# Optimization experiments

Measured on AMD Instinct MI355X. Metric: run time of the kernel, lower is better.

The kernel has to match this reference:

```python
import jax, jax.numpy as jnp
import numpy as np

N = 131072      # num nodes
T = 16          # tile (block) size, tile_rows == tile_cols
BR = N // T     # block rows = 8192
K = 8           # nonzero blocks per block-row
IN_F, HID, NCLS = 128, 256, 64
LN_EPS = 1e-5


def setup_inputs() -> dict:
    key = jax.random.key(0)
    ks = jax.random.split(key, 8)
    features = jax.random.normal(ks[0], (N, IN_F), dtype=jnp.float32)
    block_vals = jax.random.uniform(ks[1], (BR, K, T, T), dtype=jnp.float32) / (K * T)
    block_cols = jax.random.randint(ks[2], (BR, K), 0, BR, dtype=jnp.int32)
    W0 = jax.random.normal(ks[3], (IN_F, HID), dtype=jnp.float32) / np.sqrt(IN_F)
    W1 = jax.random.normal(ks[4], (HID, HID), dtype=jnp.float32) / np.sqrt(HID)
    W2 = jax.random.normal(ks[5], (HID, NCLS), dtype=jnp.float32) / np.sqrt(HID)
    return {
        "features": features,
        "block_vals": block_vals,
        "W0": W0, "b0": jnp.zeros((HID,), jnp.float32),
        "W1": W1, "b1": jnp.zeros((HID,), jnp.float32),
        "W2": W2, "b2": jnp.zeros((NCLS,), jnp.float32),
        "g0": jnp.ones((HID,), jnp.float32), "beta0": jnp.zeros((HID,), jnp.float32),
        "g1": jnp.ones((HID,), jnp.float32), "beta1": jnp.zeros((HID,), jnp.float32),
        "block_cols": block_cols,
    }


def bcsr_spmm(block_vals, block_cols, z):
    """Block-CSR sparse matmul: out = A @ z.
    block_vals: [BR, K, T, T], block_cols: [BR, K] (block-column ids), z: [N, F]."""
    f = z.shape[-1]
    zb = z.reshape(BR, T, f)[block_cols]          # gather column blocks -> [BR, K, T, F]
    out = jnp.einsum('bkrc,bkcf->brf', block_vals, zb)  # block GEMM + accumulate over K
    return out.reshape(N, f)


def layer_norm(x, g, b):
    mu = jnp.mean(x, axis=-1, keepdims=True)
    var = jnp.mean(jnp.square(x - mu), axis=-1, keepdims=True)
    return g * (x - mu) * jax.lax.rsqrt(var + LN_EPS) + b


def reference(features, block_vals, W0, b0, W1, b1, W2, b2,
              g0, beta0, g1, beta1, block_cols):
    # layer 0: h' = A @ (h W0) + b0 ; relu ; LayerNorm
    h = bcsr_spmm(block_vals, block_cols, features @ W0) + b0
    h = layer_norm(jax.nn.relu(h), g0, beta0)
    # layer 1
    h = bcsr_spmm(block_vals, block_cols, h @ W1) + b1
    h = layer_norm(jax.nn.relu(h), g1, beta1)
    # output layer (no activation/norm)
    h = bcsr_spmm(block_vals, block_cols, h @ W2) + b2
    return h
```

## Files before the change

kernel.cpp:

```cpp
#include <hip/hip_runtime.h>
#include <hip/hip_bf16.h>


typedef __bf16 bf16;
typedef bf16 bf16x8 __attribute__((ext_vector_type(8)));
typedef bf16 bf16x4 __attribute__((ext_vector_type(4)));
typedef float f32x4 __attribute__((ext_vector_type(4)));

#define N_NODES 131072
#define BRQ 8192
#define KNZ 8
#define IN_F 128
#define HID 256
#define NCLS 64
#define NROWS 8

#define SB() __builtin_amdgcn_sched_barrier(0)

static __device__ __forceinline__ f32x4 mfma16(bf16x8 a, bf16x8 b, f32x4 c) {
  return __builtin_amdgcn_mfma_f32_16x16x32_bf16(a, b, c, 0, 0, 0);
}

static __device__ __forceinline__ bf16x8 cvt8(f32x4 a0, f32x4 a1) {
  bf16x8 r;
  r[0] = (bf16)a0[0]; r[1] = (bf16)a0[1]; r[2] = (bf16)a0[2]; r[3] = (bf16)a0[3];
  r[4] = (bf16)a1[0]; r[5] = (bf16)a1[1]; r[6] = (bf16)a1[2]; r[7] = (bf16)a1[3];
  return r;
}

__global__ __launch_bounds__(256) void prep_fbt(const float* __restrict__ F,
                                                bf16* __restrict__ out) {
  __shared__ float T[16][132];
  const int b = blockIdx.x, tid = threadIdx.x;
#pragma unroll
  for (int p = 0; p < 2; ++p) {
    int ci = tid + p * 256;
    int r = ci >> 5, c4 = ci & 31;
    f32x4 v = *(const f32x4*)(F + ((long)b * 16 + r) * 128 + c4 * 4);
    *(f32x4*)&T[r][c4 * 4] = v;
  }
  __syncthreads();
  int f = tid >> 1, r0 = (tid & 1) * 8;
  bf16x8 o;
#pragma unroll
  for (int e = 0; e < 8; ++e) o[e] = (bf16)T[r0 + e][f];
  *(bf16x8*)(out + (long)b * 2048 + f * 16 + r0) = o;
}

template<int F_IN, int F_OUT, int WAVES, bool LN>
__global__ __launch_bounds__(WAVES * 64, 2) void fused_layer(
    const float* __restrict__ Abv, const int* __restrict__ Abc,
    const bf16* __restrict__ Xbt, const float* __restrict__ W,
    const float* __restrict__ bias, const float* __restrict__ gamma,
    const float* __restrict__ beta, bf16* __restrict__ Hbt,
    float* __restrict__ Out) {
  constexpr int TS = F_IN / (16 * WAVES);
  constexpr int TD = F_OUT / (16 * WAVES);
  constexpr int KD = F_IN / 32;
  constexpr int RW = F_IN + 8;
  constexpr long XBLK = (long)F_IN * 32;

  const int wave = threadIdx.x >> 6;
  const int lane = threadIdx.x & 63;
  const int l15 = lane & 15, quad = lane >> 4;
  const int cst = (quad & 1) * 8, half = quad >> 1;
  const int fsl = wave * 16 * TS;
  const int nb  = wave * 16 * TD;

  __shared__ bf16 Sh[2][16][RW];
  __shared__ float LS[WAVES][16], LSS[WAVES][16];

  bf16x8 wbf[KD][TD];
#pragma unroll
  for (int kp = 0; kp < KD; ++kp)
#pragma unroll
    for (int t = 0; t < TD; ++t) {
      const float* wp = W + (long)(kp * 32 + quad * 8) * F_OUT + nb + t * 16 + l15;
      bf16x8 v;
#pragma unroll
      for (int j = 0; j < 8; ++j) v[j] = (bf16)wp[(long)j * F_OUT];
      wbf[kp][t] = v;
    }
  float bv[TD], gv[TD], btv[TD];
#pragma unroll
  for (int t = 0; t < TD; ++t) {
    int n = nb + t * 16 + l15;
    bv[t] = bias[n];
    if constexpr (LN) { gv[t] = gamma[n]; btv[t] = beta[n]; }
  }

  const int b0 = blockIdx.x * NROWS;
  const char* zb = (const char*)Xbt;
  const unsigned fo0 = (unsigned)((fsl + l15) * 32 + cst * 2);

  int bcc[4];
  bf16x8 bfr[4][TS];
  f32x4 araw[4][2];
  {
    const int* bc = Abc + b0 * KNZ;
#pragma unroll
    for (int kp = 0; kp < 4; ++kp) {
      long zo = (long)bc[2 * kp + half] * XBLK;
#pragma unroll
      for (int t = 0; t < TS; ++t)
        bfr[kp][t] = *(const bf16x8*)(zb + zo + fo0 + (unsigned)t * 512);
    }
    const float* ab = Abv + (long)b0 * (KNZ * 256) + l15 * 16 + cst;
#pragma unroll
    for (int kp = 0; kp < 4; ++kp) {
      const float* p = ab + (2 * kp + half) * 256;
      araw[kp][0] = *(const f32x4*)p;
      araw[kp][1] = *(const f32x4*)(p + 4);
    }
    if (NROWS > 1) {
      const int* bc1 = Abc + (b0 + 1) * KNZ;
#pragma unroll
      for (int kp = 0; kp < 4; ++kp) bcc[kp] = bc1[2 * kp + half];
    }
  }

#pragma unroll
  for (int it = 0; it < NROWS; ++it) {
    const int b = b0 + it;
    bf16x8 afr[4];
#pragma unroll
    for (int kp = 0; kp < 4; ++kp) afr[kp] = cvt8(araw[kp][0], araw[kp][1]);
    int bcn[4];
    if (it + 2 < NROWS) {
      const int* bc = Abc + (b + 2) * KNZ;
#pragma unroll
      for (int kp = 0; kp < 4; ++kp) bcn[kp] = bc[2 * kp + half];
    }
    f32x4 sacc[TS] = {};
#pragma unroll
    for (int kp = 0; kp < 4; ++kp)
#pragma unroll
      for (int t = 0; t < TS; ++t)
        sacc[t] = mfma16(afr[kp], bfr[kp][t], sacc[t]);
    SB();
#pragma unroll
    for (int t = 0; t < TS; ++t) {
      int f = fsl + t * 16 + l15;
#pragma unroll
      for (int i = 0; i < 4; ++i) {
        float s = sacc[t][i];
        bf16 hi = (bf16)s;
        bf16 lo = (bf16)(s - (float)hi);
        int r = quad * 4 + i;
        Sh[0][r][f] = hi;
        Sh[1][r][f] = lo;
      }
    }
    SB();
    if (it + 1 < NROWS) {
#pragma unroll
      for (int kp = 0; kp < 4; ++kp) {
        long zo = (long)bcc[kp] * XBLK;
#pragma unroll
        for (int t = 0; t < TS; ++t)
          bfr[kp][t] = *(const bf16x8*)(zb + zo + fo0 + (unsigned)t * 512);
      }
      const float* ab = Abv + (long)(b + 1) * (KNZ * 256) + l15 * 16 + cst;
#pragma unroll
      for (int kp = 0; kp < 4; ++kp) {
        const float* p = ab + (2 * kp + half) * 256;
        araw[kp][0] = *(const f32x4*)p;
        araw[kp][1] = *(const f32x4*)(p + 4);
      }
      if (it + 2 < NROWS) {
#pragma unroll
        for (int kp = 0; kp < 4; ++kp) bcc[kp] = bcn[kp];
      }
    }
    SB();
    asm volatile("s_waitcnt lgkmcnt(0)" ::: "memory");
    __builtin_amdgcn_s_barrier();
    SB();
    f32x4 dacc[TD] = {};
#pragma unroll
    for (int kp = 0; kp < KD; ++kp) {
      bf16x8 shi = *(const bf16x8*)&Sh[0][l15][kp * 32 + quad * 8];
      bf16x8 slo = *(const bf16x8*)&Sh[1][l15][kp * 32 + quad * 8];
#pragma unroll
      for (int t = 0; t < TD; ++t) {
        dacc[t] = mfma16(shi, wbf[kp][t], dacc[t]);
        dacc[t] = mfma16(slo, wbf[kp][t], dacc[t]);
      }
    }
    SB();
    if constexpr (LN) {
      float ps[4] = {0.f, 0.f, 0.f, 0.f}, pss[4] = {0.f, 0.f, 0.f, 0.f};
#pragma unroll
      for (int t = 0; t < TD; ++t)
#pragma unroll
        for (int i = 0; i < 4; ++i) {
          float v = dacc[t][i] + bv[t];
          v = v > 0.f ? v : 0.f;
          dacc[t][i] = v;
          ps[i] += v;
          pss[i] += v * v;
        }
#pragma unroll
      for (int m = 1; m < 16; m <<= 1)
#pragma unroll
        for (int i = 0; i < 4; ++i) {
          ps[i]  += __shfl_xor(ps[i], m, 64);
          pss[i] += __shfl_xor(pss[i], m, 64);
        }
      if (l15 == 0)
#pragma unroll
        for (int i = 0; i < 4; ++i) {
          LS[wave][quad * 4 + i]  = ps[i];
          LSS[wave][quad * 4 + i] = pss[i];
        }
      SB();
      asm volatile("s_waitcnt lgkmcnt(0)" ::: "memory");
      __builtin_amdgcn_s_barrier();
      SB();
      float mu[4], rstd[4];
#pragma unroll
      for (int i = 0; i < 4; ++i) {
        int r = quad * 4 + i;
        float s = 0.f, ss = 0.f;
#pragma unroll
        for (int w = 0; w < WAVES; ++w) { s += LS[w][r]; ss += LSS[w][r]; }
        mu[i] = s * (1.f / F_OUT);
        float var = ss * (1.f / F_OUT) - mu[i] * mu[i];
        rstd[i] = rsqrtf(var + 1e-5f);
      }
      bf16* hb = Hbt + (long)b * (F_OUT * 16);
#pragma unroll
      for (int t = 0; t < TD; ++t) {
        int n = nb + t * 16 + l15;
        bf16x4 o;
#pragma unroll
        for (int i = 0; i < 4; ++i)
          o[i] = (bf16)((dacc[t][i] - mu[i]) * rstd[i] * gv[t] + btv[t]);
        *(bf16x4*)(hb + n * 16 + quad * 4) = o;
      }
    } else {
#pragma unroll
      for (int t = 0; t < TD; ++t) {
        int n = nb + t * 16 + l15;
#pragma unroll
        for (int i = 0; i < 4; ++i)
          Out[((long)b * 16 + quad * 4 + i) * NCLS + n] = dacc[t][i] + bv[t];
      }
    }
    SB();
  }
}

extern "C" void kernel_launch(void* const* d_in, const int* in_sizes, int n_in,
                              void* d_out, int out_size, void* d_ws, size_t ws_size,
                              hipStream_t stream) {
  const float* features = (const float*)d_in[0];
  const float* bvals    = (const float*)d_in[1];
  const float* W0       = (const float*)d_in[2];
  const float* b0       = (const float*)d_in[3];
  const float* W1       = (const float*)d_in[4];
  const float* b1       = (const float*)d_in[5];
  const float* W2       = (const float*)d_in[6];
  const float* b2       = (const float*)d_in[7];
  const float* g0       = (const float*)d_in[8];
  const float* beta0    = (const float*)d_in[9];
  const float* g1       = (const float*)d_in[10];
  const float* beta1    = (const float*)d_in[11];
  const int*   bcols    = (const int*)d_in[12];
  float* outp = (float*)d_out;

  bf16* fbt = (bf16*)d_ws;
  bf16* hB  = (bf16*)d_ws;
  bf16* hA  = (bf16*)d_ws + (size_t)N_NODES * HID;

  prep_fbt<<<dim3(BRQ), dim3(256), 0, stream>>>(features, fbt);
  fused_layer<IN_F, HID, 8, true><<<dim3(BRQ / NROWS), dim3(512), 0, stream>>>(
      bvals, bcols, fbt, W0, b0, g0, beta0, hA, nullptr);
  fused_layer<HID, HID, 8, true><<<dim3(BRQ / NROWS), dim3(512), 0, stream>>>(
      bvals, bcols, hA, W1, b1, g1, beta1, hB, nullptr);
  fused_layer<HID, NCLS, 4, false><<<dim3(BRQ / NROWS), dim3(256), 0, stream>>>(
      bvals, bcols, hB, W2, b2, nullptr, nullptr, nullptr, outp);
}
```

Baseline: 463.9 us.

## Restructure fused layer: batch 8 SpMM rows into LDS, one dense row-tile per wave

The SpMM results for all 8 block-rows are staged in shared memory first, using a two-slot register prefetch of the gathered feature and A tiles. Each wave then does the full dense GEMM for one block-row, reading weights pre-transposed to bf16 in a small extra kernel. This removes the per-row block barrier and the cross-wave LayerNorm reduction, and drops the hi/lo bf16 split, halving the dense MFMA count at some precision cost. Weights are now streamed from global memory instead of held in registers. The transposed weights are written into the output buffer as scratch, which the last layer later overwrites.

```diff
diff --git a/kernel.cpp b/kernel.cpp
--- a/kernel.cpp
+++ b/kernel.cpp
@@ -13,9 +13,6 @@
 #define IN_F 128
 #define HID 256
 #define NCLS 64
-#define NROWS 8
-
-#define SB() __builtin_amdgcn_sched_barrier(0)
 
 static __device__ __forceinline__ f32x4 mfma16(bf16x8 a, bf16x8 b, f32x4 c) {
   return __builtin_amdgcn_mfma_f32_16x16x32_bf16(a, b, c, 0, 0, 0);
@@ -28,6 +25,20 @@
   return r;
 }
 
+__global__ __launch_bounds__(256) void transpose_all(const float* __restrict__ W0,
+                                                     const float* __restrict__ W1,
+                                                     bf16* __restrict__ w0t,
+                                                     bf16* __restrict__ w1t) {
+  int idx = blockIdx.x * 256 + threadIdx.x;
+  if (idx < 32768) {
+    int r = idx >> 8, c = idx & 255;
+    w0t[c * 128 + r] = (bf16)W0[idx];
+  } else {
+    int j = idx - 32768; int r = j >> 8, c = j & 255;
+    w1t[c * 256 + r] = (bf16)W1[j];
+  }
+}
+
 __global__ __launch_bounds__(256) void prep_fbt(const float* __restrict__ F,
                                                 bf16* __restrict__ out) {
   __shared__ float T[16][132];
@@ -47,207 +58,165 @@
   *(bf16x8*)(out + (long)b * 2048 + f * 16 + r0) = o;
 }
 
-template<int F_IN, int F_OUT, int WAVES, bool LN>
-__global__ __launch_bounds__(WAVES * 64, 2) void fused_layer(
+template<int F_IN, int F_OUT, bool IS_OUT>
+__global__ __launch_bounds__(512, 2) void fused_v2(
     const float* __restrict__ Abv, const int* __restrict__ Abc,
-    const bf16* __restrict__ Xbt, const float* __restrict__ W,
-    const float* __restrict__ bias, const float* __restrict__ gamma,
-    const float* __restrict__ beta, bf16* __restrict__ Hbt,
-    float* __restrict__ Out) {
-  constexpr int TS = F_IN / (16 * WAVES);
-  constexpr int TD = F_OUT / (16 * WAVES);
+    const bf16* __restrict__ Xbt, const bf16* __restrict__ WT,
+    const float* __restrict__ W2, const float* __restrict__ bias,
+    const float* __restrict__ gamma, const float* __restrict__ beta,
+    bf16* __restrict__ Hbt, float* __restrict__ Out) {
+  constexpr int TS = F_IN / 128;
   constexpr int KD = F_IN / 32;
+  constexpr int T2 = F_OUT / 16;
   constexpr int RW = F_IN + 8;
   constexpr long XBLK = (long)F_IN * 32;
 
   const int wave = threadIdx.x >> 6;
   const int lane = threadIdx.x & 63;
-  const int l15 = lane & 15, quad = lane >> 4;
-  const int cst = (quad & 1) * 8, half = quad >> 1;
+  const int l15 = lane & 15, q = lane >> 4;
+  const int cst = (q & 1) * 8, half = q >> 1;
   const int fsl = wave * 16 * TS;
-  const int nb  = wave * 16 * TD;
-
-  __shared__ bf16 Sh[2][16][RW];
-  __shared__ float LS[WAVES][16], LSS[WAVES][16];
-
-  bf16x8 wbf[KD][TD];
-#pragma unroll
-  for (int kp = 0; kp < KD; ++kp)
-#pragma unroll
-    for (int t = 0; t < TD; ++t) {
-      const float* wp = W + (long)(kp * 32 + quad * 8) * F_OUT + nb + t * 16 + l15;
-      bf16x8 v;
-#pragma unroll
-      for (int j = 0; j < 8; ++j) v[j] = (bf16)wp[(long)j * F_OUT];
-      wbf[kp][t] = v;
-    }
-  float bv[TD], gv[TD], btv[TD];
-#pragma unroll
-  for (int t = 0; t < TD; ++t) {
-    int n = nb + t * 16 + l15;
-    bv[t] = bias[n];
-    if constexpr (LN) { gv[t] = gamma[n]; btv[t] = beta[n]; }
-  }
-
-  const int b0 = blockIdx.x * NROWS;
+
+  __shared__ bf16 Sar[8 * 16 * RW];
+
+  const int b0 = blockIdx.x * 8;
   const char* zb = (const char*)Xbt;
   const unsigned fo0 = (unsigned)((fsl + l15) * 32 + cst * 2);
 
-  int bcc[4];
-  bf16x8 bfr[4][TS];
-  f32x4 araw[4][2];
-  {
-    const int* bc = Abc + b0 * KNZ;
+  int bca[8][4];
+#pragma unroll
+  for (int rr = 0; rr < 8; ++rr)
+#pragma unroll
+    for (int kp = 0; kp < 4; ++kp)
+      bca[rr][kp] = Abc[(b0 + rr) * KNZ + 2 * kp + half];
+
+  bf16x8 bfr[2][4][TS];
+  f32x4  ar[2][4][2];
+
+  auto issue = [&](int rr, int slot) {
+    const float* ab = Abv + (long)(b0 + rr) * (KNZ * 256) + l15 * 16 + cst;
 #pragma unroll
     for (int kp = 0; kp < 4; ++kp) {
-      long zo = (long)bc[2 * kp + half] * XBLK;
+      const char* src = zb + (long)bca[rr][kp] * XBLK + fo0;
 #pragma unroll
       for (int t = 0; t < TS; ++t)
-        bfr[kp][t] = *(const bf16x8*)(zb + zo + fo0 + (unsigned)t * 512);
-    }
-    const float* ab = Abv + (long)b0 * (KNZ * 256) + l15 * 16 + cst;
-#pragma unroll
-    for (int kp = 0; kp < 4; ++kp) {
+        bfr[slot][kp][t] = *(const bf16x8*)(src + (unsigned)t * 512);
       const float* p = ab + (2 * kp + half) * 256;
-      araw[kp][0] = *(const f32x4*)p;
-      araw[kp][1] = *(const f32x4*)(p + 4);
-    }
-    if (NROWS > 1) {
-      const int* bc1 = Abc + (b0 + 1) * KNZ;
-#pragma unroll
-      for (int kp = 0; kp < 4; ++kp) bcc[kp] = bc1[2 * kp + half];
-    }
-  }
-
-#pragma unroll
-  for (int it = 0; it < NROWS; ++it) {
-    const int b = b0 + it;
+      ar[slot][kp][0] = *(const f32x4*)p;
+      ar[slot][kp][1] = *(const f32x4*)(p + 4);
+    }
+  };
+  issue(0, 0);
+  issue(1, 1);
+
+#pragma unroll
+  for (int r = 0; r < 8; ++r) {
+    const int slot = r & 1;
     bf16x8 afr[4];
 #pragma unroll
-    for (int kp = 0; kp < 4; ++kp) afr[kp] = cvt8(araw[kp][0], araw[kp][1]);
-    int bcn[4];
-    if (it + 2 < NROWS) {
-      const int* bc = Abc + (b + 2) * KNZ;
-#pragma unroll
-      for (int kp = 0; kp < 4; ++kp) bcn[kp] = bc[2 * kp + half];
-    }
+    for (int kp = 0; kp < 4; ++kp) afr[kp] = cvt8(ar[slot][kp][0], ar[slot][kp][1]);
     f32x4 sacc[TS] = {};
 #pragma unroll
     for (int kp = 0; kp < 4; ++kp)
 #pragma unroll
       for (int t = 0; t < TS; ++t)
-        sacc[t] = mfma16(afr[kp], bfr[kp][t], sacc[t]);
-    SB();
+        sacc[t] = mfma16(bfr[slot][kp][t], afr[kp], sacc[t]);
 #pragma unroll
     for (int t = 0; t < TS; ++t) {
-      int f = fsl + t * 16 + l15;
+      bf16x4 sv;
+#pragma unroll
+      for (int i = 0; i < 4; ++i) sv[i] = (bf16)sacc[t][i];
+      *(bf16x4*)&Sar[(r * 16 + l15) * RW + fsl + 16 * t + 4 * q] = sv;
+    }
+    if (r + 2 < 8) issue(r + 2, slot);
+  }
+
+  __syncthreads();
+
+  const int rb = wave;
+
+  if constexpr (!IS_OUT) {
+    float bv[T2], gv[T2], btv[T2];
+#pragma unroll
+    for (int t = 0; t < T2; ++t) {
+      int n = 16 * t + l15;
+      bv[t] = bias[n]; gv[t] = gamma[n]; btv[t] = beta[n];
+    }
+    f32x4 dacc[T2] = {};
+#pragma unroll
+    for (int kp = 0; kp < KD; ++kp) {
+      bf16x8 sa = *(const bf16x8*)&Sar[(rb * 16 + l15) * RW + 32 * kp + 8 * q];
+      const bf16* wb = WT + 32 * kp + 8 * q + (long)l15 * F_IN;
+#pragma unroll
+      for (int t = 0; t < T2; ++t) {
+        bf16x8 wf = *(const bf16x8*)(wb + (long)(16 * t) * F_IN);
+        dacc[t] = mfma16(sa, wf, dacc[t]);
+      }
+    }
+    float ps[4] = {0.f, 0.f, 0.f, 0.f}, pss[4] = {0.f, 0.f, 0.f, 0.f};
+#pragma unroll
+    for (int t = 0; t < T2; ++t)
 #pragma unroll
       for (int i = 0; i < 4; ++i) {
-        float s = sacc[t][i];
-        bf16 hi = (bf16)s;
-        bf16 lo = (bf16)(s - (float)hi);
-        int r = quad * 4 + i;
-        Sh[0][r][f] = hi;
-        Sh[1][r][f] = lo;
-      }
-    }
-    SB();
-    if (it + 1 < NROWS) {
-#pragma unroll
-      for (int kp = 0; kp < 4; ++kp) {
-        long zo = (long)bcc[kp] * XBLK;
-#pragma unroll
-        for (int t = 0; t < TS; ++t)
-          bfr[kp][t] = *(const bf16x8*)(zb + zo + fo0 + (unsigned)t * 512);
-      }
-      const float* ab = Abv + (long)(b + 1) * (KNZ * 256) + l15 * 16 + cst;
-#pragma unroll
-      for (int kp = 0; kp < 4; ++kp) {
-        const float* p = ab + (2 * kp + half) * 256;
-        araw[kp][0] = *(const f32x4*)p;
-        araw[kp][1] = *(const f32x4*)(p + 4);
-      }
-      if (it + 2 < NROWS) {
-#pragma unroll
-        for (int kp = 0; kp < 4; ++kp) bcc[kp] = bcn[kp];
-      }
-    }
-    SB();
-    asm volatile("s_waitcnt lgkmcnt(0)" ::: "memory");
-    __builtin_amdgcn_s_barrier();
-    SB();
-    f32x4 dacc[TD] = {};
+        float v = dacc[t][i] + bv[t];
+        v = v > 0.f ? v : 0.f;
+        dacc[t][i] = v;
+        ps[i] += v;
+        pss[i] += v * v;
+      }
+#pragma unroll
+    for (int m = 1; m < 16; m <<= 1)
+#pragma unroll
+      for (int i = 0; i < 4; ++i) {
+        ps[i]  += __shfl_xor(ps[i], m, 64);
+        pss[i] += __shfl_xor(pss[i], m, 64);
+      }
+    float mu[4], rstd[4];
+#pragma unroll
+    for (int i = 0; i < 4; ++i) {
+      mu[i] = ps[i] * (1.f / F_OUT);
+      float var = pss[i] * (1.f / F_OUT) - mu[i] * mu[i];
+      rstd[i] = rsqrtf(var + 1e-5f);
+    }
+    bf16* hb = Hbt + (long)(b0 + rb) * (F_OUT * 16);
+#pragma unroll
+    for (int t = 0; t < T2; ++t) {
+      bf16x4 o;
+#pragma unroll
+      for (int i = 0; i < 4; ++i)
+        o[i] = (bf16)((dacc[t][i] - mu[i]) * rstd[i] * gv[t] + btv[t]);
+      *(bf16x4*)(hb + (16 * t + l15) * 16 + 4 * q) = o;
+    }
+  } else {
+    bf16x8 wf2[KD][T2];
+#pragma unroll
+    for (int kp = 0; kp < KD; ++kp)
+#pragma unroll
+      for (int t = 0; t < T2; ++t) {
+        const float* wp = W2 + (long)(32 * kp + 8 * q) * F_OUT + 16 * t + l15;
+        bf16x8 v;
+#pragma unroll
+        for (int j = 0; j < 8; ++j) v[j] = (bf16)wp[(long)j * F_OUT];
+        wf2[kp][t] = v;
+      }
+    float bv[T2];
+#pragma unroll
+    for (int t = 0; t < T2; ++t) bv[t] = bias[16 * t + l15];
+    f32x4 dacc[T2] = {};
 #pragma unroll
     for (int kp = 0; kp < KD; ++kp) {
-      bf16x8 shi = *(const bf16x8*)&Sh[0][l15][kp * 32 + quad * 8];
-      bf16x8 slo = *(const bf16x8*)&Sh[1][l15][kp * 32 + quad * 8];
-#pragma unroll
-      for (int t = 0; t < TD; ++t) {
-        dacc[t] = mfma16(shi, wbf[kp][t], dacc[t]);
-        dacc[t] = mfma16(slo, wbf[kp][t], dacc[t]);
-      }
-    }
-    SB();
-    if constexpr (LN) {
-      float ps[4] = {0.f, 0.f, 0.f, 0.f}, pss[4] = {0.f, 0.f, 0.f, 0.f};
-#pragma unroll
-      for (int t = 0; t < TD; ++t)
-#pragma unroll
-        for (int i = 0; i < 4; ++i) {
-          float v = dacc[t][i] + bv[t];
-          v = v > 0.f ? v : 0.f;
-          dacc[t][i] = v;
-          ps[i] += v;
-          pss[i] += v * v;
-        }
-#pragma unroll
-      for (int m = 1; m < 16; m <<= 1)
-#pragma unroll
-        for (int i = 0; i < 4; ++i) {
-          ps[i]  += __shfl_xor(ps[i], m, 64);
-          pss[i] += __shfl_xor(pss[i], m, 64);
-        }
-      if (l15 == 0)
-#pragma unroll
-        for (int i = 0; i < 4; ++i) {
-          LS[wave][quad * 4 + i]  = ps[i];
-          LSS[wave][quad * 4 + i] = pss[i];
-        }
-      SB();
-      asm volatile("s_waitcnt lgkmcnt(0)" ::: "memory");
-      __builtin_amdgcn_s_barrier();
-      SB();
-      float mu[4], rstd[4];
-#pragma unroll
-      for (int i = 0; i < 4; ++i) {
-        int r = quad * 4 + i;
-        float s = 0.f, ss = 0.f;
-#pragma unroll
-        for (int w = 0; w < WAVES; ++w) { s += LS[w][r]; ss += LSS[w][r]; }
-        mu[i] = s * (1.f / F_OUT);
-        float var = ss * (1.f / F_OUT) - mu[i] * mu[i];
-        rstd[i] = rsqrtf(var + 1e-5f);
-      }
-      bf16* hb = Hbt + (long)b * (F_OUT * 16);
-#pragma unroll
-      for (int t = 0; t < TD; ++t) {
-        int n = nb + t * 16 + l15;
-        bf16x4 o;
-#pragma unroll
-        for (int i = 0; i < 4; ++i)
-          o[i] = (bf16)((dacc[t][i] - mu[i]) * rstd[i] * gv[t] + btv[t]);
-        *(bf16x4*)(hb + n * 16 + quad * 4) = o;
-      }
-    } else {
-#pragma unroll
-      for (int t = 0; t < TD; ++t) {
-        int n = nb + t * 16 + l15;
-#pragma unroll
-        for (int i = 0; i < 4; ++i)
-          Out[((long)b * 16 + quad * 4 + i) * NCLS + n] = dacc[t][i] + bv[t];
-      }
-    }
-    SB();
+      bf16x8 sa = *(const bf16x8*)&Sar[(rb * 16 + l15) * RW + 32 * kp + 8 * q];
+#pragma unroll
+      for (int t = 0; t < T2; ++t)
+        dacc[t] = mfma16(sa, wf2[kp][t], dacc[t]);
+    }
+#pragma unroll
+    for (int t = 0; t < T2; ++t) {
+      int n = 16 * t + l15;
+#pragma unroll
+      for (int i = 0; i < 4; ++i)
+        Out[((long)(b0 + rb) * 16 + 4 * q + i) * NCLS + n] = dacc[t][i] + bv[t];
+    }
   }
 }
 
@@ -257,11 +226,11 @@
   const float* features = (const float*)d_in[0];
   const float* bvals    = (const float*)d_in[1];
   const float* W0       = (const float*)d_in[2];
-  const float* b0       = (const float*)d_in[3];
+  const float* b0v      = (const float*)d_in[3];
   const float* W1       = (const float*)d_in[4];
-  const float* b1       = (const float*)d_in[5];
+  const float* b1v      = (const float*)d_in[5];
   const float* W2       = (const float*)d_in[6];
-  const float* b2       = (const float*)d_in[7];
+  const float* b2v      = (const float*)d_in[7];
   const float* g0       = (const float*)d_in[8];
   const float* beta0    = (const float*)d_in[9];
   const float* g1       = (const float*)d_in[10];
@@ -273,11 +242,16 @@
   bf16* hB  = (bf16*)d_ws;
   bf16* hA  = (bf16*)d_ws + (size_t)N_NODES * HID;
 
+  bf16* w0t = (bf16*)d_out;
+  bf16* w1t = w0t + IN_F * HID;
+
+  transpose_all<<<dim3(384), dim3(256), 0, stream>>>(W0, W1, w0t, w1t);
   prep_fbt<<<dim3(BRQ), dim3(256), 0, stream>>>(features, fbt);
-  fused_layer<IN_F, HID, 8, true><<<dim3(BRQ / NROWS), dim3(512), 0, stream>>>(
-      bvals, bcols, fbt, W0, b0, g0, beta0, hA, nullptr);
-  fused_layer<HID, HID, 8, true><<<dim3(BRQ / NROWS), dim3(512), 0, stream>>>(
-      bvals, bcols, hA, W1, b1, g1, beta1, hB, nullptr);
-  fused_layer<HID, NCLS, 4, false><<<dim3(BRQ / NROWS), dim3(256), 0, stream>>>(
-      bvals, bcols, hB, W2, b2, nullptr, nullptr, nullptr, outp);
-}
+
+  fused_v2<IN_F, HID, false><<<dim3(BRQ / 8), dim3(512), 0, stream>>>(
+      bvals, bcols, fbt, w0t, nullptr, b0v, g0, beta0, hA, nullptr);
+  fused_v2<HID, HID, false><<<dim3(BRQ / 8), dim3(512), 0, stream>>>(
+      bvals, bcols, hA, w1t, nullptr, b1v, g1, beta1, hB, nullptr);
+  fused_v2<HID, NCLS, true><<<dim3(BRQ / 8), dim3(512), 0, stream>>>(
+      bvals, bcols, hB, nullptr, W2, b2v, nullptr, nullptr, nullptr, outp);
+}
```

Measured after the change: 590.2 us. 27.2% more time.
